# Optimization experiments

Hardware: AMD Instinct MI355X
Metric: run time of the kernel (lower is better)

Reference implementation:

```python
import jax, jax.numpy as jnp
import numpy as np

V = 1000      # output_dim (vocab)
H = 512       # hidden_dim
D = 512       # input_dim == d_model of MHA
HEADS = 8
DK = D // HEADS
MEM = 512     # memory_len
BS = 128      # batch
TMAX = 160    # max decode steps (== max(output_lens))


def setup_inputs() -> dict:
    key = jax.random.key(0)
    ks = jax.random.split(key, 16)
    s = 0.05
    f = lambda k, shape: jax.random.normal(k, shape, jnp.float32) * s
    memory = jax.random.normal(ks[0], (MEM, BS, D), jnp.float32)
    lens = jnp.sort(jax.random.randint(ks[1], (BS,), 1, TMAX + 1))[::-1]
    lens = lens.at[0].set(TMAX)  # torch runs max(output_lens) steps; pin to TMAX
    return dict(
        memory=memory,
        emb=f(ks[2], (V, H)),
        Wq=f(ks[3], (D, 2 * H)), bq=f(ks[4], (D,)),
        Wk=f(ks[5], (D, D)), bk=f(ks[6], (D,)),
        Wv=f(ks[7], (D, D)), bv=f(ks[8], (D,)),
        W_ih=f(ks[9], (3 * H, D)), W_hh=f(ks[10], (3 * H, H)),
        b_ih=f(ks[11], (3 * H,)), b_hh=f(ks[12], (3 * H,)),
        Wfc=f(ks[13], (V, H)), bfc=f(ks[14], (V,)),
        output_lens=lens,
    )


def _forward(memory, emb, Wq, bq, Wk, bk, Wv, bv, W_ih, W_hh, b_ih, b_hh, Wfc, bfc, output_lens):
    mem_len, bs, _ = memory.shape
    scale = 1.0 / np.sqrt(DK)
    # Precompute key/value projections once (memory is constant over decode steps).
    # (mem_len, bs, D) -> (bs, heads, mem_len, dk)
    kp = (memory @ Wk.T + bk).reshape(mem_len, bs, HEADS, DK).transpose(1, 2, 0, 3)
    vp = (memory @ Wv.T + bv).reshape(mem_len, bs, HEADS, DK).transpose(1, 2, 0, 3)

    def step(carry, i):
        out, hid = carry  # (bs, V), (bs, H)
        tok = jnp.argmax(out, axis=-1)                 # greedy feedback (annotations=None)
        q = jnp.concatenate([emb[tok], hid], axis=-1) @ Wq.T + bq  # (bs, D)
        qh = q.reshape(bs, HEADS, DK)
        att = jax.nn.softmax(jnp.einsum('bhd,bhmd->bhm', qh, kp) * scale, axis=-1)
        ctx = jnp.einsum('bhm,bhmd->bhd', att, vp).reshape(bs, D)
        # GRU cell (PyTorch gate order: r, z, n)
        gi = ctx @ W_ih.T + b_ih
        gh = hid @ W_hh.T + b_hh
        ir, iz, inn = jnp.split(gi, 3, axis=-1)
        hr, hz, hn = jnp.split(gh, 3, axis=-1)
        r = jax.nn.sigmoid(ir + hr)
        z = jax.nn.sigmoid(iz + hz)
        n = jnp.tanh(inn + r * hn)
        h_new = (1.0 - z) * n + z * hid
        o_new = h_new @ Wfc.T + bfc
        # Ragged masking: torch truncates finished batch items; each item is
        # independent, so masking the recorded outputs is equivalent.
        run = (i < output_lens)[:, None]
        ys = (jnp.where(run, o_new, 0.0),
              jnp.where(run, h_new, 0.0),
              jnp.where(run, att.mean(axis=1), 0.0))
        return (o_new, h_new), ys

    init = (jnp.zeros((bs, V), jnp.float32), jnp.zeros((bs, H), jnp.float32))
    _, (outputs, hiddens, scores) = jax.lax.scan(step, init, jnp.arange(TMAX))
    return outputs, hiddens, scores  # (T,bs,V), (T,bs,H), (T,bs,mem_len)


def reference(memory, emb, Wq, bq, Wk, bk, Wv, bv, W_ih, W_hh, b_ih, b_hh, Wfc, bfc, output_lens):
    return _forward(memory, emb, Wq, bq, Wk, bk, Wv, bv, W_ih, W_hh, b_ih, b_hh, Wfc, bfc, output_lens)
```

## Files before the change

kernel.cpp:

```cpp
#include <hip/hip_runtime.h>
#include <hip/hip_fp16.h>
#include <math.h>

__global__ __launch_bounds__(256) void kv_proj(
    const float* __restrict__ mem, const float* __restrict__ W,
    const float* __restrict__ bias, __half* __restrict__ outp) {
  __shared__ float As[32][68];
  __shared__ float Bs[32][68];
  int gid = blockIdx.x;
  int jt = gid & 7, mt = (gid >> 3) & 7, b = gid >> 6;
  int t = threadIdx.x;
  int lm = t >> 2;
  int kq = (t & 3) * 8;
  int tx = t & 15, ty = t >> 4;
  float acc[4][4];
  #pragma unroll
  for (int r = 0; r < 4; ++r)
    #pragma unroll
    for (int c = 0; c < 4; ++c) acc[r][c] = 0.f;
  const float* Arow = mem + (size_t)(mt * 64 + lm) * 65536 + (size_t)b * 512 + kq;
  const float* Brow = W + (size_t)(jt * 64 + lm) * 512 + kq;
  for (int k0 = 0; k0 < 512; k0 += 32) {
    float4 a0 = *(const float4*)(Arow + k0);
    float4 a1 = *(const float4*)(Arow + k0 + 4);
    float4 b0 = *(const float4*)(Brow + k0);
    float4 b1 = *(const float4*)(Brow + k0 + 4);
    As[kq + 0][lm] = a0.x; As[kq + 1][lm] = a0.y; As[kq + 2][lm] = a0.z; As[kq + 3][lm] = a0.w;
    As[kq + 4][lm] = a1.x; As[kq + 5][lm] = a1.y; As[kq + 6][lm] = a1.z; As[kq + 7][lm] = a1.w;
    Bs[kq + 0][lm] = b0.x; Bs[kq + 1][lm] = b0.y; Bs[kq + 2][lm] = b0.z; Bs[kq + 3][lm] = b0.w;
    Bs[kq + 4][lm] = b1.x; Bs[kq + 5][lm] = b1.y; Bs[kq + 6][lm] = b1.z; Bs[kq + 7][lm] = b1.w;
    __syncthreads();
    #pragma unroll
    for (int k = 0; k < 32; ++k) {
      float4 av = *(const float4*)&As[k][ty * 4];
      float4 bv = *(const float4*)&Bs[k][tx * 4];
      float ar[4] = {av.x, av.y, av.z, av.w};
      float br[4] = {bv.x, bv.y, bv.z, bv.w};
      #pragma unroll
      for (int r = 0; r < 4; ++r)
        #pragma unroll
        for (int c = 0; c < 4; ++c) acc[r][c] = fmaf(ar[r], br[c], acc[r][c]);
    }
    __syncthreads();
  }
  float4 bb = *(const float4*)(bias + jt * 64 + tx * 4);
  #pragma unroll
  for (int r = 0; r < 4; ++r) {
    int m = mt * 64 + ty * 4 + r;
    __half2 p0 = __floats2half2_rn(acc[r][0] + bb.x, acc[r][1] + bb.y);
    __half2 p1 = __floats2half2_rn(acc[r][2] + bb.z, acc[r][3] + bb.w);
    union { uint2 u; __half2 h[2]; } W2;
    W2.h[0] = p0; W2.h[1] = p1;
    *(uint2*)(outp + (((size_t)b * 8 + jt) * 512 + m) * 64 + tx * 4) = W2.u;
  }
}

__global__ __launch_bounds__(256) void kv_projT(
    const float* __restrict__ mem, const float* __restrict__ W,
    const float* __restrict__ bias, __half* __restrict__ outp) {
  __shared__ float As[32][68];
  __shared__ float Bs[32][68];
  int gid = blockIdx.x;
  int jt = gid & 7, mt = (gid >> 3) & 7, b = gid >> 6;
  int t = threadIdx.x;
  int lm = t >> 2;
  int kq = (t & 3) * 8;
  int tx = t & 15, ty = t >> 4;
  float acc[4][4];
  #pragma unroll
  for (int r = 0; r < 4; ++r)
    #pragma unroll
    for (int c = 0; c < 4; ++c) acc[r][c] = 0.f;
  const float* Arow = mem + (size_t)(mt * 64 + lm) * 65536 + (size_t)b * 512 + kq;
  const float* Brow = W + (size_t)(jt * 64 + lm) * 512 + kq;
  for (int k0 = 0; k0 < 512; k0 += 32) {
    float4 a0 = *(const float4*)(Arow + k0);
    float4 a1 = *(const float4*)(Arow + k0 + 4);
    float4 b0 = *(const float4*)(Brow + k0);
    float4 b1 = *(const float4*)(Brow + k0 + 4);
    As[kq + 0][lm] = a0.x; As[kq + 1][lm] = a0.y; As[kq + 2][lm] = a0.z; As[kq + 3][lm] = a0.w;
    As[kq + 4][lm] = a1.x; As[kq + 5][lm] = a1.y; As[kq + 6][lm] = a1.z; As[kq + 7][lm] = a1.w;
    Bs[kq + 0][lm] = b0.x; Bs[kq + 1][lm] = b0.y; Bs[kq + 2][lm] = b0.z; Bs[kq + 3][lm] = b0.w;
    Bs[kq + 4][lm] = b1.x; Bs[kq + 5][lm] = b1.y; Bs[kq + 6][lm] = b1.z; Bs[kq + 7][lm] = b1.w;
    __syncthreads();
    #pragma unroll
    for (int k = 0; k < 32; ++k) {
      float4 av = *(const float4*)&As[k][ty * 4];
      float4 bv = *(const float4*)&Bs[k][tx * 4];
      float ar[4] = {av.x, av.y, av.z, av.w};
      float br[4] = {bv.x, bv.y, bv.z, bv.w};
      #pragma unroll
      for (int r = 0; r < 4; ++r)
        #pragma unroll
        for (int c = 0; c < 4; ++c) acc[r][c] = fmaf(ar[r], br[c], acc[r][c]);
    }
    __syncthreads();
  }
  float4 bb = *(const float4*)(bias + jt * 64 + tx * 4);
  float bc[4] = {bb.x, bb.y, bb.z, bb.w};
  #pragma unroll
  for (int r = 0; r < 4; ++r) {
    int m = mt * 64 + ty * 4 + r;
    #pragma unroll
    for (int c = 0; c < 4; ++c) {
      int d = tx * 4 + c;
      outp[((size_t)(b * 8 + jt) * 64 + d) * 512 + m] = __float2half_rn(acc[r][c] + bc[c]);
    }
  }
}

__global__ __launch_bounds__(256) void e2_kernel(
    const float* __restrict__ emb, const float* __restrict__ Wq,
    const float* __restrict__ bq, float* __restrict__ E2) {
  __shared__ float As[32][68];
  __shared__ float Bs[32][68];
  int gid = blockIdx.x;
  int jt = gid & 7, mt = gid >> 3;
  int t = threadIdx.x;
  int lm = t >> 2;
  int kq = (t & 3) * 8;
  int tx = t & 15, ty = t >> 4;
  float acc[4][4];
  #pragma unroll
  for (int r = 0; r < 4; ++r)
    #pragma unroll
    for (int c = 0; c < 4; ++c) acc[r][c] = 0.f;
  int v = mt * 64 + lm;
  bool aok = v < 1000;
  const float* Arow = emb + (size_t)v * 512 + kq;
  const float* Brow = Wq + (size_t)(jt * 64 + lm) * 1024 + kq;
  for (int k0 = 0; k0 < 512; k0 += 32) {
    float4 a0, a1;
    if (aok) {
      a0 = *(const float4*)(Arow + k0);
      a1 = *(const float4*)(Arow + k0 + 4);
    } else {
      a0 = make_float4(0.f, 0.f, 0.f, 0.f);
      a1 = make_float4(0.f, 0.f, 0.f, 0.f);
    }
    float4 b0 = *(const float4*)(Brow + k0);
    float4 b1 = *(const float4*)(Brow + k0 + 4);
    As[kq + 0][lm] = a0.x; As[kq + 1][lm] = a0.y; As[kq + 2][lm] = a0.z; As[kq + 3][lm] = a0.w;
    As[kq + 4][lm] = a1.x; As[kq + 5][lm] = a1.y; As[kq + 6][lm] = a1.z; As[kq + 7][lm] = a1.w;
    Bs[kq + 0][lm] = b0.x; Bs[kq + 1][lm] = b0.y; Bs[kq + 2][lm] = b0.z; Bs[kq + 3][lm] = b0.w;
    Bs[kq + 4][lm] = b1.x; Bs[kq + 5][lm] = b1.y; Bs[kq + 6][lm] = b1.z; Bs[kq + 7][lm] = b1.w;
    __syncthreads();
    #pragma unroll
    for (int k = 0; k < 32; ++k) {
      float4 av = *(const float4*)&As[k][ty * 4];
      float4 bv = *(const float4*)&Bs[k][tx * 4];
      float ar[4] = {av.x, av.y, av.z, av.w};
      float br[4] = {bv.x, bv.y, bv.z, bv.w};
      #pragma unroll
      for (int r = 0; r < 4; ++r)
        #pragma unroll
        for (int c = 0; c < 4; ++c) acc[r][c] = fmaf(ar[r], br[c], acc[r][c]);
    }
    __syncthreads();
  }
  float4 bb = *(const float4*)(bq + jt * 64 + tx * 4);
  float bc[4] = {bb.x, bb.y, bb.z, bb.w};
  #pragma unroll
  for (int r = 0; r < 4; ++r) {
    int vv = mt * 64 + ty * 4 + r;
    if (vv < 1000) {
      #pragma unroll
      for (int c = 0; c < 4; ++c)
        E2[(size_t)vv * 512 + jt * 64 + tx * 4 + c] = acc[r][c] + bc[c];
    }
  }
}

__global__ __launch_bounds__(256) void init_kernel(float* __restrict__ h0,
                                                   float* __restrict__ qh,
                                                   unsigned long long* __restrict__ packed) {
  int t = threadIdx.x + blockIdx.x * blockDim.x;
  for (int i = t; i < 128 * 512; i += blockDim.x * gridDim.x) {
    h0[i] = 0.f;
    qh[i] = 0.f;
  }
  if (t < 128) packed[t] = (0x80000000ull << 32) | 0xFFFFFFFFull;
}

__global__ __launch_bounds__(256) void attn_fused(
    const __half* __restrict__ kpT, const __half* __restrict__ vp,
    const float* __restrict__ E2, const float* __restrict__ qh,
    const unsigned long long* __restrict__ packed,
    float* __restrict__ ctx, float* __restrict__ att_buf) {
  int b = blockIdx.x >> 3, hd = blockIdx.x & 7;
  __shared__ float qs[64];
  __shared__ float att[512];
  __shared__ __align__(16) float red[16][68];
  __shared__ float rmax[4], rsum[4];
  __shared__ int tok_s;
  int t = threadIdx.x;
  if (t == 0) tok_s = (int)(0xFFFFFFFFu - (unsigned int)(packed[b] & 0xFFFFFFFFull));
  __syncthreads();
  int tok = tok_s;
  if (t < 64)
    qs[t] = qh[(size_t)b * 512 + hd * 64 + t] + E2[(size_t)tok * 512 + hd * 64 + t];
  __syncthreads();

  const __half* Kb = kpT + (size_t)(b * 8 + hd) * 32768;
  float s0 = 0.f, s1 = 0.f;
  {
    int m2 = 2 * t;
    #pragma unroll 16
    for (int d = 0; d < 64; ++d) {
      __half2 kk = *(const __half2*)(Kb + (size_t)d * 512 + m2);
      float2 kf = __half22float2(kk);
      float qd = qs[d];
      s0 = fmaf(qd, kf.x, s0);
      s1 = fmaf(qd, kf.y, s1);
    }
    s0 *= 0.125f;
    s1 *= 0.125f;
  }
  float mx = fmaxf(s0, s1);
  #pragma unroll
  for (int o = 32; o > 0; o >>= 1) mx = fmaxf(mx, __shfl_xor(mx, o));
  if ((t & 63) == 0) rmax[t >> 6] = mx;
  __syncthreads();
  mx = fmaxf(fmaxf(rmax[0], rmax[1]), fmaxf(rmax[2], rmax[3]));
  float e0 = expf(s0 - mx), e1 = expf(s1 - mx);
  float sm = e0 + e1;
  #pragma unroll
  for (int o = 32; o > 0; o >>= 1) sm += __shfl_xor(sm, o);
  if ((t & 63) == 0) rsum[t >> 6] = sm;
  __syncthreads();
  sm = rsum[0] + rsum[1] + rsum[2] + rsum[3];
  float inv = 1.f / sm;
  float a0 = e0 * inv, a1 = e1 * inv;
  att[2 * t] = a0;
  att[2 * t + 1] = a1;
  *(float2*)(att_buf + (size_t)(b * 8 + hd) * 512 + 2 * t) = make_float2(a0, a1);
  __syncthreads();

  const __half* Vb = vp + (size_t)(b * 8 + hd) * 32768;
  {
    int dsl = (t & 15) * 4, g = t >> 4;
    float c0 = 0.f, c1 = 0.f, c2 = 0.f, c3 = 0.f;
    #pragma unroll 8
    for (int m = g; m < 512; m += 16) {
      union { uint2 u; __half2 h[2]; } U;
      U.u = *(const uint2*)(Vb + (size_t)m * 64 + dsl);
      float2 f01 = __half22float2(U.h[0]);
      float2 f23 = __half22float2(U.h[1]);
      float am = att[m];
      c0 = fmaf(am, f01.x, c0);
      c1 = fmaf(am, f01.y, c1);
      c2 = fmaf(am, f23.x, c2);
      c3 = fmaf(am, f23.y, c3);
    }
    red[g][dsl + 0] = c0;
    red[g][dsl + 1] = c1;
    red[g][dsl + 2] = c2;
    red[g][dsl + 3] = c3;
  }
  __syncthreads();
  if (t < 64) {
    float cc = 0.f;
    #pragma unroll
    for (int g2 = 0; g2 < 16; ++g2) cc += red[g2][t];
    ctx[(size_t)b * 512 + hd * 64 + t] = cc;
  }
}

__global__ __launch_bounds__(256) void gru_kernel(
    const float* __restrict__ W_ih, const float* __restrict__ W_hh,
    const float* __restrict__ b_ih, const float* __restrict__ b_hh,
    const float* __restrict__ ctx, const float* __restrict__ h_prev,
    float* __restrict__ h_new, const float* __restrict__ att_buf,
    const int* __restrict__ lens, float* __restrict__ out_hid,
    float* __restrict__ out_sc, unsigned long long* __restrict__ packed,
    int step) {
  __shared__ float cs[8][512];
  __shared__ float hs[8][512];
  int bi = blockIdx.x;
  int t = threadIdx.x;
  if (bi >= 256) {
    int sb = bi - 256;
    if (sb == 0 && t < 128) packed[t] = 0ull;
    #pragma unroll
    for (int i = 0; i < 4; ++i) {
      int flat = sb * 1024 + i * 256 + t;
      int bb = flat >> 9, m = flat & 511;
      float sum = 0.f;
      #pragma unroll
      for (int h = 0; h < 8; ++h) sum += att_buf[(size_t)(bb * 8 + h) * 512 + m];
      float val = sum * 0.125f;
      out_sc[(size_t)step * 65536 + flat] = (step < lens[bb]) ? val : 0.f;
    }
    return;
  }
  int bt = bi >> 4, jt = bi & 15;
  #pragma unroll
  for (int i = 0; i < 16; ++i) {
    int flat = i * 256 + t;
    int lb = flat >> 9, k = flat & 511;
    cs[lb][k] = ctx[(size_t)(bt * 8 + lb) * 512 + k];
    hs[lb][k] = h_prev[(size_t)(bt * 8 + lb) * 512 + k];
  }
  __syncthreads();
  int lb = t >> 5, j = (jt << 5) + (t & 31);
  int b = bt * 8 + lb;
  float air = b_ih[j], aiz = b_ih[512 + j], ain = b_ih[1024 + j];
  float ahr = b_hh[j], ahz = b_hh[512 + j], ahn = b_hh[1024 + j];
  const float* c = cs[lb];
  const float* hh = hs[lb];
  const float* wi0 = W_ih + (size_t)j * 512;
  const float* wi1 = W_ih + (size_t)(512 + j) * 512;
  const float* wi2 = W_ih + (size_t)(1024 + j) * 512;
  const float* wh0 = W_hh + (size_t)j * 512;
  const float* wh1 = W_hh + (size_t)(512 + j) * 512;
  const float* wh2 = W_hh + (size_t)(1024 + j) * 512;
  #pragma unroll 2
  for (int k = 0; k < 512; k += 4) {
    float4 wa = *(const float4*)(wi0 + k);
    float4 wb = *(const float4*)(wi1 + k);
    float4 wc = *(const float4*)(wi2 + k);
    float4 wd = *(const float4*)(wh0 + k);
    float4 we = *(const float4*)(wh1 + k);
    float4 wf = *(const float4*)(wh2 + k);
    float c0 = c[k], c1 = c[k + 1], c2 = c[k + 2], c3 = c[k + 3];
    float h0 = hh[k], h1 = hh[k + 1], h2 = hh[k + 2], h3 = hh[k + 3];
    air = fmaf(c0, wa.x, air); air = fmaf(c1, wa.y, air); air = fmaf(c2, wa.z, air); air = fmaf(c3, wa.w, air);
    aiz = fmaf(c0, wb.x, aiz); aiz = fmaf(c1, wb.y, aiz); aiz = fmaf(c2, wb.z, aiz); aiz = fmaf(c3, wb.w, aiz);
    ain = fmaf(c0, wc.x, ain); ain = fmaf(c1, wc.y, ain); ain = fmaf(c2, wc.z, ain); ain = fmaf(c3, wc.w, ain);
    ahr = fmaf(h0, wd.x, ahr); ahr = fmaf(h1, wd.y, ahr); ahr = fmaf(h2, wd.z, ahr); ahr = fmaf(h3, wd.w, ahr);
    ahz = fmaf(h0, we.x, ahz); ahz = fmaf(h1, we.y, ahz); ahz = fmaf(h2, we.z, ahz); ahz = fmaf(h3, we.w, ahz);
    ahn = fmaf(h0, wf.x, ahn); ahn = fmaf(h1, wf.y, ahn); ahn = fmaf(h2, wf.z, ahn); ahn = fmaf(h3, wf.w, ahn);
  }
  float r = 1.f / (1.f + expf(-(air + ahr)));
  float z = 1.f / (1.f + expf(-(aiz + ahz)));
  float n = tanhf(fmaf(r, ahn, ain));
  float hp = hh[j];
  float hv = (1.f - z) * n + z * hp;
  h_new[(size_t)b * 512 + j] = hv;
  out_hid[(size_t)step * 65536 + (size_t)b * 512 + j] = (step < lens[b]) ? hv : 0.f;
}

__global__ __launch_bounds__(256) void logits_kernel(
    const float* __restrict__ Wfc, const float* __restrict__ bfc,
    const float* __restrict__ h_new, const int* __restrict__ lens,
    float* __restrict__ out_o, unsigned long long* __restrict__ packed,
    const float* __restrict__ Wq, float* __restrict__ qh, int step) {
  __shared__ float hs[8][512];
  int bi = blockIdx.x;
  int t = threadIdx.x;
  int bt = bi >> 4, vt = bi & 15;
  #pragma unroll
  for (int i = 0; i < 16; ++i) {
    int flat = i * 256 + t;
    int lb = flat >> 9, k = flat & 511;
    hs[lb][k] = h_new[(size_t)(bt * 8 + lb) * 512 + k];
  }
  __syncthreads();
  int lb = t >> 5, vv = t & 31;
  int b = bt * 8 + lb;
  const float* a = hs[lb];
  int run = step < lens[b];
  float bestv = -1e30f;
  int besti = 0;
  #pragma unroll
  for (int r = 0; r < 2; ++r) {
    int v = vt * 64 + r * 32 + vv;
    if (v < 1000) {
      float acc = bfc[v];
      const float* wrow = Wfc + (size_t)v * 512;
      #pragma unroll 4
      for (int k = 0; k < 512; k += 4) {
        float4 w = *(const float4*)(wrow + k);
        acc = fmaf(a[k + 0], w.x, acc);
        acc = fmaf(a[k + 1], w.y, acc);
        acc = fmaf(a[k + 2], w.z, acc);
        acc = fmaf(a[k + 3], w.w, acc);
      }
      out_o[(size_t)step * 128000 + (size_t)b * 1000 + v] = run ? acc : 0.f;
      if (acc > bestv) { bestv = acc; besti = v; }
    }
  }
  #pragma unroll
  for (int o = 16; o > 0; o >>= 1) {
    float ov = __shfl_xor(bestv, o);
    int oi = __shfl_xor(besti, o);
    if (ov > bestv || (ov == bestv && oi < besti)) { bestv = ov; besti = oi; }
  }
  if (vv == 0) {
    unsigned int fb = __float_as_uint(bestv);
    fb = (fb & 0x80000000u) ? ~fb : (fb | 0x80000000u);
    unsigned long long key =
        ((unsigned long long)fb << 32) | (unsigned long long)(0xFFFFFFFFu - (unsigned int)besti);
    atomicMax(packed + b, key);
  }

  {
    int jq = vt * 32 + (t & 31);
    const float* wrow = Wq + (size_t)jq * 1024 + 512;
    float acc = 0.f;
    #pragma unroll 4
    for (int k = 0; k < 512; k += 4) {
      float4 w = *(const float4*)(wrow + k);
      acc = fmaf(a[k + 0], w.x, acc);
      acc = fmaf(a[k + 1], w.y, acc);
      acc = fmaf(a[k + 2], w.z, acc);
      acc = fmaf(a[k + 3], w.w, acc);
    }
    qh[(size_t)b * 512 + jq] = acc;
  }
}

extern "C" void kernel_launch(void* const* d_in, const int* in_sizes, int n_in,
                              void* d_out, int out_size, void* d_ws, size_t ws_size,
                              hipStream_t stream) {
  const float* memory = (const float*)d_in[0];
  const float* emb    = (const float*)d_in[1];
  const float* Wq     = (const float*)d_in[2];
  const float* bq     = (const float*)d_in[3];
  const float* Wk     = (const float*)d_in[4];
  const float* bk     = (const float*)d_in[5];
  const float* Wv     = (const float*)d_in[6];
  const float* bv     = (const float*)d_in[7];
  const float* W_ih   = (const float*)d_in[8];
  const float* W_hh   = (const float*)d_in[9];
  const float* b_ih   = (const float*)d_in[10];
  const float* b_hh   = (const float*)d_in[11];
  const float* Wfc    = (const float*)d_in[12];
  const float* bfc    = (const float*)d_in[13];
  const int* lens     = (const int*)d_in[14];

  __half* kpT = (__half*)d_ws;
  __half* vp  = kpT + 33554432;
  float* ctx     = (float*)(vp + 33554432);
  float* h0      = ctx + 65536;
  float* h1      = h0 + 65536;
  float* qh      = h1 + 65536;
  float* E2      = qh + 65536;
  float* att_buf = E2 + 512000;
  unsigned long long* packed = (unsigned long long*)(att_buf + 524288);

  float* out   = (float*)d_out;
  float* out_o = out;
  float* out_h = out + 20480000;
  float* out_s = out_h + 10485760;

  kv_projT<<<8192, 256, 0, stream>>>(memory, Wk, bk, kpT);
  kv_proj<<<8192, 256, 0, stream>>>(memory, Wv, bv, vp);
  e2_kernel<<<128, 256, 0, stream>>>(emb, Wq, bq, E2);
  init_kernel<<<64, 256, 0, stream>>>(h0, qh, packed);

  for (int t = 0; t < 160; ++t) {
    float* hp = (t & 1) ? h1 : h0;
    float* hn = (t & 1) ? h0 : h1;
    attn_fused<<<1024, 256, 0, stream>>>(kpT, vp, E2, qh, packed, ctx, att_buf);
    gru_kernel<<<320, 256, 0, stream>>>(W_ih, W_hh, b_ih, b_hh, ctx, hp, hn,
                                        att_buf, lens, out_h, out_s, packed, t);
    logits_kernel<<<256, 256, 0, stream>>>(Wfc, bfc, hn, lens, out_o, packed, Wq, qh, t);
  }
}
```

Before: 25.94 ms.

## Fuse decode loop into one persistent cooperative kernel with grid syncs

Replaces the 480 per-step kernel launches (attention, GRU, logits) with a single cooperative persistent kernel of 512 blocks that loops over the 160 steps and separates phases with grid-wide syncs. Each block handles two batch-head attention tiles per step, and a subset of blocks then runs the GRU and logits phases. The goal is to remove launch overhead and inter-kernel gaps. The cost is lower parallelism in the attention phase (1024 tiles on 512 blocks) and grid.sync overhead. The old multi-kernel loop stays as a fallback if the cooperative launch fails.

```diff
diff --git a/kernel.cpp b/kernel.cpp
--- a/kernel.cpp
+++ b/kernel.cpp
@@ -1,6 +1,9 @@
 #include <hip/hip_runtime.h>
 #include <hip/hip_fp16.h>
+#include <hip/hip_cooperative_groups.h>
 #include <math.h>
+
+namespace cg = cooperative_groups;
 
 __global__ __launch_bounds__(256) void kv_proj(
     const float* __restrict__ mem, const float* __restrict__ W,
@@ -200,7 +203,6 @@
   if (t < 64)
     qs[t] = qh[(size_t)b * 512 + hd * 64 + t] + E2[(size_t)tok * 512 + hd * 64 + t];
   __syncthreads();
-
   const __half* Kb = kpT + (size_t)(b * 8 + hd) * 32768;
   float s0 = 0.f, s1 = 0.f;
   {
@@ -235,7 +237,6 @@
   att[2 * t + 1] = a1;
   *(float2*)(att_buf + (size_t)(b * 8 + hd) * 512 + 2 * t) = make_float2(a0, a1);
   __syncthreads();
-
   const __half* Vb = vp + (size_t)(b * 8 + hd) * 32768;
   {
     int dsl = (t & 15) * 4, g = t >> 4;
@@ -393,7 +394,6 @@
         ((unsigned long long)fb << 32) | (unsigned long long)(0xFFFFFFFFu - (unsigned int)besti);
     atomicMax(packed + b, key);
   }
-
   {
     int jq = vt * 32 + (t & 31);
     const float* wrow = Wq + (size_t)jq * 1024 + 512;
@@ -407,6 +407,249 @@
       acc = fmaf(a[k + 3], w.w, acc);
     }
     qh[(size_t)b * 512 + jq] = acc;
+  }
+}
+
+__global__ __launch_bounds__(256, 2) void decode_kernel(
+    const __half* __restrict__ kpT, const __half* __restrict__ vp,
+    const float* __restrict__ E2, float* __restrict__ qh,
+    float* __restrict__ h0, float* __restrict__ h1,
+    float* __restrict__ ctx, float* __restrict__ att_buf,
+    unsigned long long* __restrict__ packed,
+    const float* __restrict__ W_ih, const float* __restrict__ W_hh,
+    const float* __restrict__ b_ih, const float* __restrict__ b_hh,
+    const float* __restrict__ Wfc, const float* __restrict__ bfc,
+    const float* __restrict__ Wq, const int* __restrict__ lens,
+    float* __restrict__ out_o, float* __restrict__ out_h,
+    float* __restrict__ out_s) {
+  cg::grid_group grid = cg::this_grid();
+  __shared__ __align__(16) float smem[8192];
+  __shared__ int tok_s;
+  int g = blockIdx.x;
+  int t = threadIdx.x;
+
+  {
+    int idx = g * 256 + t;
+    if (idx < 65536) { h0[idx] = 0.f; qh[idx] = 0.f; }
+    if (idx < 128) packed[idx] = (0x80000000ull << 32) | 0xFFFFFFFFull;
+  }
+  grid.sync();
+
+  for (int step = 0; step < 160; ++step) {
+    const float* hp = (step & 1) ? h1 : h0;
+    float* hn = (step & 1) ? h0 : h1;
+
+    #pragma unroll 1
+    for (int p = 0; p < 2; ++p) {
+      int id = (g << 1) | p;
+      int b = id >> 3, hd = id & 7;
+      float* qs = smem;
+      float* att = smem + 64;
+      float (*red)[68] = reinterpret_cast<float(*)[68]>(smem + 576);
+      float* rmax = smem + 1664;
+      float* rsum = smem + 1668;
+
+      if (t == 0) tok_s = (int)(0xFFFFFFFFu - (unsigned int)(packed[b] & 0xFFFFFFFFull));
+      __syncthreads();
+      int tok = tok_s;
+      if (t < 64)
+        qs[t] = qh[(size_t)b * 512 + hd * 64 + t] + E2[(size_t)tok * 512 + hd * 64 + t];
+      __syncthreads();
+
+      const __half* Kb = kpT + (size_t)(b * 8 + hd) * 32768;
+      float s0 = 0.f, s1 = 0.f;
+      {
+        int m2 = 2 * t;
+        #pragma unroll 16
+        for (int d = 0; d < 64; ++d) {
+          __half2 kk = *(const __half2*)(Kb + (size_t)d * 512 + m2);
+          float2 kf = __half22float2(kk);
+          float qd = qs[d];
+          s0 = fmaf(qd, kf.x, s0);
+          s1 = fmaf(qd, kf.y, s1);
+        }
+        s0 *= 0.125f;
+        s1 *= 0.125f;
+      }
+      float mx = fmaxf(s0, s1);
+      #pragma unroll
+      for (int o = 32; o > 0; o >>= 1) mx = fmaxf(mx, __shfl_xor(mx, o));
+      if ((t & 63) == 0) rmax[t >> 6] = mx;
+      __syncthreads();
+      mx = fmaxf(fmaxf(rmax[0], rmax[1]), fmaxf(rmax[2], rmax[3]));
+      float e0 = expf(s0 - mx), e1 = expf(s1 - mx);
+      float sm = e0 + e1;
+      #pragma unroll
+      for (int o = 32; o > 0; o >>= 1) sm += __shfl_xor(sm, o);
+      if ((t & 63) == 0) rsum[t >> 6] = sm;
+      __syncthreads();
+      sm = rsum[0] + rsum[1] + rsum[2] + rsum[3];
+      float inv = 1.f / sm;
+      float a0 = e0 * inv, a1 = e1 * inv;
+      att[2 * t] = a0;
+      att[2 * t + 1] = a1;
+      *(float2*)(att_buf + (size_t)(b * 8 + hd) * 512 + 2 * t) = make_float2(a0, a1);
+      __syncthreads();
+
+      const __half* Vb = vp + (size_t)(b * 8 + hd) * 32768;
+      {
+        int dsl = (t & 15) * 4, g4 = t >> 4;
+        float c0 = 0.f, c1 = 0.f, c2 = 0.f, c3 = 0.f;
+        #pragma unroll 8
+        for (int m = g4; m < 512; m += 16) {
+          union { uint2 u; __half2 h[2]; } U;
+          U.u = *(const uint2*)(Vb + (size_t)m * 64 + dsl);
+          float2 f01 = __half22float2(U.h[0]);
+          float2 f23 = __half22float2(U.h[1]);
+          float am = att[m];
+          c0 = fmaf(am, f01.x, c0);
+          c1 = fmaf(am, f01.y, c1);
+          c2 = fmaf(am, f23.x, c2);
+          c3 = fmaf(am, f23.y, c3);
+        }
+        red[g4][dsl + 0] = c0;
+        red[g4][dsl + 1] = c1;
+        red[g4][dsl + 2] = c2;
+        red[g4][dsl + 3] = c3;
+      }
+      __syncthreads();
+      if (t < 64) {
+        float cc = 0.f;
+        #pragma unroll
+        for (int g2 = 0; g2 < 16; ++g2) cc += red[g2][t];
+        ctx[(size_t)b * 512 + hd * 64 + t] = cc;
+      }
+      __syncthreads();
+    }
+    grid.sync();
+
+    if (g < 256) {
+      float (*cs)[512] = reinterpret_cast<float(*)[512]>(smem);
+      float (*hs)[512] = reinterpret_cast<float(*)[512]>(smem + 4096);
+      int bt = g >> 4, jt = g & 15;
+      #pragma unroll
+      for (int i = 0; i < 16; ++i) {
+        int flat = i * 256 + t;
+        int lb = flat >> 9, k = flat & 511;
+        cs[lb][k] = ctx[(size_t)(bt * 8 + lb) * 512 + k];
+        hs[lb][k] = hp[(size_t)(bt * 8 + lb) * 512 + k];
+      }
+      __syncthreads();
+      int lb = t >> 5, j = (jt << 5) + (t & 31);
+      int b = bt * 8 + lb;
+      float air = b_ih[j], aiz = b_ih[512 + j], ain = b_ih[1024 + j];
+      float ahr = b_hh[j], ahz = b_hh[512 + j], ahn = b_hh[1024 + j];
+      const float* c = cs[lb];
+      const float* hh = hs[lb];
+      const float* wi0 = W_ih + (size_t)j * 512;
+      const float* wi1 = W_ih + (size_t)(512 + j) * 512;
+      const float* wi2 = W_ih + (size_t)(1024 + j) * 512;
+      const float* wh0 = W_hh + (size_t)j * 512;
+      const float* wh1 = W_hh + (size_t)(512 + j) * 512;
+      const float* wh2 = W_hh + (size_t)(1024 + j) * 512;
+      #pragma unroll 2
+      for (int k = 0; k < 512; k += 4) {
+        float4 wa = *(const float4*)(wi0 + k);
+        float4 wb = *(const float4*)(wi1 + k);
+        float4 wc = *(const float4*)(wi2 + k);
+        float4 wd = *(const float4*)(wh0 + k);
+        float4 we = *(const float4*)(wh1 + k);
+        float4 wf = *(const float4*)(wh2 + k);
+        float c0 = c[k], c1 = c[k + 1], c2 = c[k + 2], c3 = c[k + 3];
+        float h0v = hh[k], h1v = hh[k + 1], h2v = hh[k + 2], h3v = hh[k + 3];
+        air = fmaf(c0, wa.x, air); air = fmaf(c1, wa.y, air); air = fmaf(c2, wa.z, air); air = fmaf(c3, wa.w, air);
+        aiz = fmaf(c0, wb.x, aiz); aiz = fmaf(c1, wb.y, aiz); aiz = fmaf(c2, wb.z, aiz); aiz = fmaf(c3, wb.w, aiz);
+        ain = fmaf(c0, wc.x, ain); ain = fmaf(c1, wc.y, ain); ain = fmaf(c2, wc.z, ain); ain = fmaf(c3, wc.w, ain);
+        ahr = fmaf(h0v, wd.x, ahr); ahr = fmaf(h1v, wd.y, ahr); ahr = fmaf(h2v, wd.z, ahr); ahr = fmaf(h3v, wd.w, ahr);
+        ahz = fmaf(h0v, we.x, ahz); ahz = fmaf(h1v, we.y, ahz); ahz = fmaf(h2v, we.z, ahz); ahz = fmaf(h3v, we.w, ahz);
+        ahn = fmaf(h0v, wf.x, ahn); ahn = fmaf(h1v, wf.y, ahn); ahn = fmaf(h2v, wf.z, ahn); ahn = fmaf(h3v, wf.w, ahn);
+      }
+      float r = 1.f / (1.f + expf(-(air + ahr)));
+      float z = 1.f / (1.f + expf(-(aiz + ahz)));
+      float n = tanhf(fmaf(r, ahn, ain));
+      float hpv = hh[j];
+      float hv = (1.f - z) * n + z * hpv;
+      hn[(size_t)b * 512 + j] = hv;
+      out_h[(size_t)step * 65536 + (size_t)b * 512 + j] = (step < lens[b]) ? hv : 0.f;
+    } else if (g < 320) {
+      int sb = g - 256;
+      if (sb == 0 && t < 128) packed[t] = 0ull;
+      #pragma unroll
+      for (int i = 0; i < 4; ++i) {
+        int flat = sb * 1024 + i * 256 + t;
+        int bb = flat >> 9, m = flat & 511;
+        float sum = 0.f;
+        #pragma unroll
+        for (int h = 0; h < 8; ++h) sum += att_buf[(size_t)(bb * 8 + h) * 512 + m];
+        float val = sum * 0.125f;
+        out_s[(size_t)step * 65536 + flat] = (step < lens[bb]) ? val : 0.f;
+      }
+    }
+    grid.sync();
+
+    if (g < 256) {
+      float (*hs)[512] = reinterpret_cast<float(*)[512]>(smem);
+      int bt = g >> 4, vt = g & 15;
+      #pragma unroll
+      for (int i = 0; i < 16; ++i) {
+        int flat = i * 256 + t;
+        int lb = flat >> 9, k = flat & 511;
+        hs[lb][k] = hn[(size_t)(bt * 8 + lb) * 512 + k];
+      }
+      __syncthreads();
+      int lb = t >> 5, vv = t & 31;
+      int b = bt * 8 + lb;
+      const float* a = hs[lb];
+      int run = step < lens[b];
+      float bestv = -1e30f;
+      int besti = 0;
+      #pragma unroll
+      for (int r = 0; r < 2; ++r) {
+        int v = vt * 64 + r * 32 + vv;
+        if (v < 1000) {
+          float acc = bfc[v];
+          const float* wrow = Wfc + (size_t)v * 512;
+          #pragma unroll 4
+          for (int k = 0; k < 512; k += 4) {
+            float4 w = *(const float4*)(wrow + k);
+            acc = fmaf(a[k + 0], w.x, acc);
+            acc = fmaf(a[k + 1], w.y, acc);
+            acc = fmaf(a[k + 2], w.z, acc);
+            acc = fmaf(a[k + 3], w.w, acc);
+          }
+          out_o[(size_t)step * 128000 + (size_t)b * 1000 + v] = run ? acc : 0.f;
+          if (acc > bestv) { bestv = acc; besti = v; }
+        }
+      }
+      #pragma unroll
+      for (int o = 16; o > 0; o >>= 1) {
+        float ov = __shfl_xor(bestv, o);
+        int oi = __shfl_xor(besti, o);
+        if (ov > bestv || (ov == bestv && oi < besti)) { bestv = ov; besti = oi; }
+      }
+      if (vv == 0) {
+        unsigned int fb = __float_as_uint(bestv);
+        fb = (fb & 0x80000000u) ? ~fb : (fb | 0x80000000u);
+        unsigned long long key =
+            ((unsigned long long)fb << 32) | (unsigned long long)(0xFFFFFFFFu - (unsigned int)besti);
+        atomicMax(packed + b, key);
+      }
+      {
+        int jq = vt * 32 + (t & 31);
+        const float* wrow = Wq + (size_t)jq * 1024 + 512;
+        float acc = 0.f;
+        #pragma unroll 4
+        for (int k = 0; k < 512; k += 4) {
+          float4 w = *(const float4*)(wrow + k);
+          acc = fmaf(a[k + 0], w.x, acc);
+          acc = fmaf(a[k + 1], w.y, acc);
+          acc = fmaf(a[k + 2], w.z, acc);
+          acc = fmaf(a[k + 3], w.w, acc);
+        }
+        qh[(size_t)b * 512 + jq] = acc;
+      }
+    }
+    grid.sync();
   }
 }
 
@@ -447,14 +690,25 @@
   kv_projT<<<8192, 256, 0, stream>>>(memory, Wk, bk, kpT);
   kv_proj<<<8192, 256, 0, stream>>>(memory, Wv, bv, vp);
   e2_kernel<<<128, 256, 0, stream>>>(emb, Wq, bq, E2);
-  init_kernel<<<64, 256, 0, stream>>>(h0, qh, packed);
-
-  for (int t = 0; t < 160; ++t) {
-    float* hp = (t & 1) ? h1 : h0;
-    float* hn = (t & 1) ? h0 : h1;
-    attn_fused<<<1024, 256, 0, stream>>>(kpT, vp, E2, qh, packed, ctx, att_buf);
-    gru_kernel<<<320, 256, 0, stream>>>(W_ih, W_hh, b_ih, b_hh, ctx, hp, hn,
-                                        att_buf, lens, out_h, out_s, packed, t);
-    logits_kernel<<<256, 256, 0, stream>>>(Wfc, bfc, hn, lens, out_o, packed, Wq, qh, t);
-  }
-}
+
+  void* args[] = {
+      (void*)&kpT, (void*)&vp, (void*)&E2, (void*)&qh, (void*)&h0, (void*)&h1,
+      (void*)&ctx, (void*)&att_buf, (void*)&packed,
+      (void*)&W_ih, (void*)&W_hh, (void*)&b_ih, (void*)&b_hh,
+      (void*)&Wfc, (void*)&bfc, (void*)&Wq, (void*)&lens,
+      (void*)&out_o, (void*)&out_h, (void*)&out_s};
+  hipError_t err = hipLaunchCooperativeKernel((void*)decode_kernel, dim3(512),
+                                              dim3(256), args, 0, stream);
+  if (err != hipSuccess) {
+    init_kernel<<<64, 256, 0, stream>>>(h0, qh, packed);
+    for (int t = 0; t < 160; ++t) {
+      float* hp = (t & 1) ? h1 : h0;
+      float* hn = (t & 1) ? h0 : h1;
+      attn_fused<<<1024, 256, 0, stream>>>(kpT, vp, E2, qh, packed, ctx, att_buf);
+      gru_kernel<<<320, 256, 0, stream>>>(W_ih, W_hh, b_ih, b_hh, ctx, hp, hn,
+                                          att_buf, lens, out_h, out_s, packed, t);
+      logits_kernel<<<256, 256, 0, stream>>>(Wfc, bfc, hn, lens, out_o, packed, Wq,
+                                             qh, t);
+    }
+  }
+}
```

Measured after the change: 55.43 ms. 114% more time.

## Fuse logits, argmax and query projection into per-batch attention kernel

Applied to the files above, without the earlier changes.

The logits/argmax/query-projection work for step t-1 moves into the start of the next step's attention kernel. That kernel now runs one 512-thread block per batch item and covers all heads, so the argmax is resolved in shared memory instead of through global atomics on a packed buffer. The attention-score mean is also folded into this kernel, which drops the att_buf round trip and a launch per step. The cost is that each block recomputes the full Wfc and Wq matvecs for its batch item, so only 128 blocks run with heavy per-block weight streaming. That means less parallelism than the previous 1024-block attention and 256-block logits grids.

```diff
diff --git a/kernel.cpp b/kernel.cpp
--- a/kernel.cpp
+++ b/kernel.cpp
@@ -171,128 +171,154 @@
   }
 }
 
-__global__ __launch_bounds__(256) void init_kernel(float* __restrict__ h0,
-                                                   float* __restrict__ qh,
-                                                   unsigned long long* __restrict__ packed) {
+__global__ __launch_bounds__(256) void init_kernel(float* __restrict__ h0) {
   int t = threadIdx.x + blockIdx.x * blockDim.x;
-  for (int i = t; i < 128 * 512; i += blockDim.x * gridDim.x) {
-    h0[i] = 0.f;
-    qh[i] = 0.f;
-  }
-  if (t < 128) packed[t] = (0x80000000ull << 32) | 0xFFFFFFFFull;
-}
-
-__global__ __launch_bounds__(256) void attn_fused(
+  for (int i = t; i < 128 * 512; i += blockDim.x * gridDim.x) h0[i] = 0.f;
+}
+
+__global__ __launch_bounds__(512) void attn_step(
     const __half* __restrict__ kpT, const __half* __restrict__ vp,
-    const float* __restrict__ E2, const float* __restrict__ qh,
-    const unsigned long long* __restrict__ packed,
-    float* __restrict__ ctx, float* __restrict__ att_buf) {
-  int b = blockIdx.x >> 3, hd = blockIdx.x & 7;
-  __shared__ float qs[64];
-  __shared__ float att[512];
-  __shared__ __align__(16) float red[16][68];
-  __shared__ float rmax[4], rsum[4];
+    const float* __restrict__ E2, const float* __restrict__ Wfc,
+    const float* __restrict__ bfc, const float* __restrict__ Wq,
+    const float* __restrict__ h_prev, const int* __restrict__ lens,
+    float* __restrict__ out_o, float* __restrict__ out_s,
+    float* __restrict__ ctx, int step) {
+  int b = blockIdx.x;
+  int t = threadIdx.x;
+  __shared__ float hs[512];
+  __shared__ float qs[512];
+  __shared__ __align__(16) float att[8][512];
+  __shared__ float redv[8];
+  __shared__ int redi[8];
   __shared__ int tok_s;
-  int t = threadIdx.x;
-  if (t == 0) tok_s = (int)(0xFFFFFFFFu - (unsigned int)(packed[b] & 0xFFFFFFFFull));
+
+  if (step > 0) {
+    hs[t] = h_prev[(size_t)b * 512 + t];
+    __syncthreads();
+    int run = (step - 1) < lens[b];
+    float bestv = -1e30f;
+    int besti = 0;
+    #pragma unroll
+    for (int s = 0; s < 2; ++s) {
+      int v = t + s * 512;
+      if (v < 1000) {
+        float acc = bfc[v];
+        const float* wrow = Wfc + (size_t)v * 512;
+        #pragma unroll 4
+        for (int k = 0; k < 512; k += 4) {
+          float4 w = *(const float4*)(wrow + k);
+          acc = fmaf(hs[k + 0], w.x, acc);
+          acc = fmaf(hs[k + 1], w.y, acc);
+          acc = fmaf(hs[k + 2], w.z, acc);
+          acc = fmaf(hs[k + 3], w.w, acc);
+        }
+        out_o[(size_t)(step - 1) * 128000 + (size_t)b * 1000 + v] = run ? acc : 0.f;
+        if (acc > bestv) { bestv = acc; besti = v; }
+      }
+    }
+    #pragma unroll
+    for (int o = 32; o > 0; o >>= 1) {
+      float ov = __shfl_xor(bestv, o);
+      int oi = __shfl_xor(besti, o);
+      if (ov > bestv || (ov == bestv && oi < besti)) { bestv = ov; besti = oi; }
+    }
+    if ((t & 63) == 0) { redv[t >> 6] = bestv; redi[t >> 6] = besti; }
+    float qhv = 0.f;
+    {
+      const float* wrow = Wq + (size_t)t * 1024 + 512;
+      #pragma unroll 4
+      for (int k = 0; k < 512; k += 4) {
+        float4 w = *(const float4*)(wrow + k);
+        qhv = fmaf(hs[k + 0], w.x, qhv);
+        qhv = fmaf(hs[k + 1], w.y, qhv);
+        qhv = fmaf(hs[k + 2], w.z, qhv);
+        qhv = fmaf(hs[k + 3], w.w, qhv);
+      }
+    }
+    __syncthreads();
+    if (t == 0) {
+      float bv = redv[0];
+      int bi = redi[0];
+      #pragma unroll
+      for (int i = 1; i < 8; ++i)
+        if (redv[i] > bv || (redv[i] == bv && redi[i] < bi)) { bv = redv[i]; bi = redi[i]; }
+      tok_s = bi;
+    }
+    __syncthreads();
+    if (step >= 160) return;
+    qs[t] = qhv + E2[(size_t)tok_s * 512 + t];
+    __syncthreads();
+  } else {
+    qs[t] = E2[t];
+    __syncthreads();
+  }
+
+  int hd = t >> 6, lane = t & 63;
+  const __half* Kb = kpT + (size_t)(b * 8 + hd) * 32768;
+  float s0[4], s1[4];
+  #pragma unroll
+  for (int i = 0; i < 4; ++i) { s0[i] = 0.f; s1[i] = 0.f; }
+  for (int d = 0; d < 64; ++d) {
+    float qd = qs[hd * 64 + d];
+    const __half* kr = Kb + (size_t)d * 512;
+    #pragma unroll
+    for (int i = 0; i < 4; ++i) {
+      __half2 kk = *(const __half2*)(kr + 2 * (lane + 64 * i));
+      float2 kf = __half22float2(kk);
+      s0[i] = fmaf(qd, kf.x, s0[i]);
+      s1[i] = fmaf(qd, kf.y, s1[i]);
+    }
+  }
+  float mx = -1e30f;
+  #pragma unroll
+  for (int i = 0; i < 4; ++i) {
+    s0[i] *= 0.125f;
+    s1[i] *= 0.125f;
+    mx = fmaxf(mx, fmaxf(s0[i], s1[i]));
+  }
+  #pragma unroll
+  for (int o = 32; o > 0; o >>= 1) mx = fmaxf(mx, __shfl_xor(mx, o));
+  float e0[4], e1[4], sm = 0.f;
+  #pragma unroll
+  for (int i = 0; i < 4; ++i) {
+    e0[i] = expf(s0[i] - mx);
+    e1[i] = expf(s1[i] - mx);
+    sm += e0[i] + e1[i];
+  }
+  #pragma unroll
+  for (int o = 32; o > 0; o >>= 1) sm += __shfl_xor(sm, o);
+  float inv = 1.f / sm;
+  #pragma unroll
+  for (int i = 0; i < 4; ++i)
+    *(float2*)&att[hd][2 * (lane + 64 * i)] = make_float2(e0[i] * inv, e1[i] * inv);
   __syncthreads();
-  int tok = tok_s;
-  if (t < 64)
-    qs[t] = qh[(size_t)b * 512 + hd * 64 + t] + E2[(size_t)tok * 512 + hd * 64 + t];
-  __syncthreads();
-
-  const __half* Kb = kpT + (size_t)(b * 8 + hd) * 32768;
-  float s0 = 0.f, s1 = 0.f;
+
   {
-    int m2 = 2 * t;
-    #pragma unroll 16
-    for (int d = 0; d < 64; ++d) {
-      __half2 kk = *(const __half2*)(Kb + (size_t)d * 512 + m2);
-      float2 kf = __half22float2(kk);
-      float qd = qs[d];
-      s0 = fmaf(qd, kf.x, s0);
-      s1 = fmaf(qd, kf.y, s1);
-    }
-    s0 *= 0.125f;
-    s1 *= 0.125f;
-  }
-  float mx = fmaxf(s0, s1);
-  #pragma unroll
-  for (int o = 32; o > 0; o >>= 1) mx = fmaxf(mx, __shfl_xor(mx, o));
-  if ((t & 63) == 0) rmax[t >> 6] = mx;
-  __syncthreads();
-  mx = fmaxf(fmaxf(rmax[0], rmax[1]), fmaxf(rmax[2], rmax[3]));
-  float e0 = expf(s0 - mx), e1 = expf(s1 - mx);
-  float sm = e0 + e1;
-  #pragma unroll
-  for (int o = 32; o > 0; o >>= 1) sm += __shfl_xor(sm, o);
-  if ((t & 63) == 0) rsum[t >> 6] = sm;
-  __syncthreads();
-  sm = rsum[0] + rsum[1] + rsum[2] + rsum[3];
-  float inv = 1.f / sm;
-  float a0 = e0 * inv, a1 = e1 * inv;
-  att[2 * t] = a0;
-  att[2 * t + 1] = a1;
-  *(float2*)(att_buf + (size_t)(b * 8 + hd) * 512 + 2 * t) = make_float2(a0, a1);
-  __syncthreads();
+    float sum2 = 0.f;
+    #pragma unroll
+    for (int h2 = 0; h2 < 8; ++h2) sum2 += att[h2][t];
+    out_s[(size_t)step * 65536 + (size_t)b * 512 + t] =
+        (step < lens[b]) ? sum2 * 0.125f : 0.f;
+  }
 
   const __half* Vb = vp + (size_t)(b * 8 + hd) * 32768;
-  {
-    int dsl = (t & 15) * 4, g = t >> 4;
-    float c0 = 0.f, c1 = 0.f, c2 = 0.f, c3 = 0.f;
-    #pragma unroll 8
-    for (int m = g; m < 512; m += 16) {
-      union { uint2 u; __half2 h[2]; } U;
-      U.u = *(const uint2*)(Vb + (size_t)m * 64 + dsl);
-      float2 f01 = __half22float2(U.h[0]);
-      float2 f23 = __half22float2(U.h[1]);
-      float am = att[m];
-      c0 = fmaf(am, f01.x, c0);
-      c1 = fmaf(am, f01.y, c1);
-      c2 = fmaf(am, f23.x, c2);
-      c3 = fmaf(am, f23.y, c3);
-    }
-    red[g][dsl + 0] = c0;
-    red[g][dsl + 1] = c1;
-    red[g][dsl + 2] = c2;
-    red[g][dsl + 3] = c3;
-  }
-  __syncthreads();
-  if (t < 64) {
-    float cc = 0.f;
-    #pragma unroll
-    for (int g2 = 0; g2 < 16; ++g2) cc += red[g2][t];
-    ctx[(size_t)b * 512 + hd * 64 + t] = cc;
-  }
+  float cc = 0.f;
+  #pragma unroll 8
+  for (int m = 0; m < 512; ++m)
+    cc = fmaf(att[hd][m], __half2float(Vb[(size_t)m * 64 + lane]), cc);
+  ctx[(size_t)b * 512 + hd * 64 + lane] = cc;
 }
 
 __global__ __launch_bounds__(256) void gru_kernel(
     const float* __restrict__ W_ih, const float* __restrict__ W_hh,
     const float* __restrict__ b_ih, const float* __restrict__ b_hh,
     const float* __restrict__ ctx, const float* __restrict__ h_prev,
-    float* __restrict__ h_new, const float* __restrict__ att_buf,
-    const int* __restrict__ lens, float* __restrict__ out_hid,
-    float* __restrict__ out_sc, unsigned long long* __restrict__ packed,
-    int step) {
+    float* __restrict__ h_new, const int* __restrict__ lens,
+    float* __restrict__ out_hid, int step) {
   __shared__ float cs[8][512];
   __shared__ float hs[8][512];
   int bi = blockIdx.x;
   int t = threadIdx.x;
-  if (bi >= 256) {
-    int sb = bi - 256;
-    if (sb == 0 && t < 128) packed[t] = 0ull;
-    #pragma unroll
-    for (int i = 0; i < 4; ++i) {
-      int flat = sb * 1024 + i * 256 + t;
-      int bb = flat >> 9, m = flat & 511;
-      float sum = 0.f;
-      #pragma unroll
-      for (int h = 0; h < 8; ++h) sum += att_buf[(size_t)(bb * 8 + h) * 512 + m];
-      float val = sum * 0.125f;
-      out_sc[(size_t)step * 65536 + flat] = (step < lens[bb]) ? val : 0.f;
-    }
-    return;
-  }
   int bt = bi >> 4, jt = bi & 15;
   #pragma unroll
   for (int i = 0; i < 16; ++i) {
@@ -340,76 +366,6 @@
   out_hid[(size_t)step * 65536 + (size_t)b * 512 + j] = (step < lens[b]) ? hv : 0.f;
 }
 
-__global__ __launch_bounds__(256) void logits_kernel(
-    const float* __restrict__ Wfc, const float* __restrict__ bfc,
-    const float* __restrict__ h_new, const int* __restrict__ lens,
-    float* __restrict__ out_o, unsigned long long* __restrict__ packed,
-    const float* __restrict__ Wq, float* __restrict__ qh, int step) {
-  __shared__ float hs[8][512];
-  int bi = blockIdx.x;
-  int t = threadIdx.x;
-  int bt = bi >> 4, vt = bi & 15;
-  #pragma unroll
-  for (int i = 0; i < 16; ++i) {
-    int flat = i * 256 + t;
-    int lb = flat >> 9, k = flat & 511;
-    hs[lb][k] = h_new[(size_t)(bt * 8 + lb) * 512 + k];
-  }
-  __syncthreads();
-  int lb = t >> 5, vv = t & 31;
-  int b = bt * 8 + lb;
-  const float* a = hs[lb];
-  int run = step < lens[b];
-  float bestv = -1e30f;
-  int besti = 0;
-  #pragma unroll
-  for (int r = 0; r < 2; ++r) {
-    int v = vt * 64 + r * 32 + vv;
-    if (v < 1000) {
-      float acc = bfc[v];
-      const float* wrow = Wfc + (size_t)v * 512;
-      #pragma unroll 4
-      for (int k = 0; k < 512; k += 4) {
-        float4 w = *(const float4*)(wrow + k);
-        acc = fmaf(a[k + 0], w.x, acc);
-        acc = fmaf(a[k + 1], w.y, acc);
-        acc = fmaf(a[k + 2], w.z, acc);
-        acc = fmaf(a[k + 3], w.w, acc);
-      }
-      out_o[(size_t)step * 128000 + (size_t)b * 1000 + v] = run ? acc : 0.f;
-      if (acc > bestv) { bestv = acc; besti = v; }
-    }
-  }
-  #pragma unroll
-  for (int o = 16; o > 0; o >>= 1) {
-    float ov = __shfl_xor(bestv, o);
-    int oi = __shfl_xor(besti, o);
-    if (ov > bestv || (ov == bestv && oi < besti)) { bestv = ov; besti = oi; }
-  }
-  if (vv == 0) {
-    unsigned int fb = __float_as_uint(bestv);
-    fb = (fb & 0x80000000u) ? ~fb : (fb | 0x80000000u);
-    unsigned long long key =
-        ((unsigned long long)fb << 32) | (unsigned long long)(0xFFFFFFFFu - (unsigned int)besti);
-    atomicMax(packed + b, key);
-  }
-
-  {
-    int jq = vt * 32 + (t & 31);
-    const float* wrow = Wq + (size_t)jq * 1024 + 512;
-    float acc = 0.f;
-    #pragma unroll 4
-    for (int k = 0; k < 512; k += 4) {
-      float4 w = *(const float4*)(wrow + k);
-      acc = fmaf(a[k + 0], w.x, acc);
-      acc = fmaf(a[k + 1], w.y, acc);
-      acc = fmaf(a[k + 2], w.z, acc);
-      acc = fmaf(a[k + 3], w.w, acc);
-    }
-    qh[(size_t)b * 512 + jq] = acc;
-  }
-}
-
 extern "C" void kernel_launch(void* const* d_in, const int* in_sizes, int n_in,
                               void* d_out, int out_size, void* d_ws, size_t ws_size,
                               hipStream_t stream) {
@@ -434,10 +390,7 @@
   float* ctx     = (float*)(vp + 33554432);
   float* h0      = ctx + 65536;
   float* h1      = h0 + 65536;
-  float* qh      = h1 + 65536;
-  float* E2      = qh + 65536;
-  float* att_buf = E2 + 512000;
-  unsigned long long* packed = (unsigned long long*)(att_buf + 524288);
+  float* E2      = h1 + 65536;
 
   float* out   = (float*)d_out;
   float* out_o = out;
@@ -447,14 +400,17 @@
   kv_projT<<<8192, 256, 0, stream>>>(memory, Wk, bk, kpT);
   kv_proj<<<8192, 256, 0, stream>>>(memory, Wv, bv, vp);
   e2_kernel<<<128, 256, 0, stream>>>(emb, Wq, bq, E2);
-  init_kernel<<<64, 256, 0, stream>>>(h0, qh, packed);
+  init_kernel<<<64, 256, 0, stream>>>(h0);
 
   for (int t = 0; t < 160; ++t) {
+    const float* hprev_attn = (t == 0) ? h0 : (((t - 1) & 1) ? h0 : h1);
+    attn_step<<<128, 512, 0, stream>>>(kpT, vp, E2, Wfc, bfc, Wq, hprev_attn,
+                                       lens, out_o, out_s, ctx, t);
     float* hp = (t & 1) ? h1 : h0;
     float* hn = (t & 1) ? h0 : h1;
-    attn_fused<<<1024, 256, 0, stream>>>(kpT, vp, E2, qh, packed, ctx, att_buf);
-    gru_kernel<<<320, 256, 0, stream>>>(W_ih, W_hh, b_ih, b_hh, ctx, hp, hn,
-                                        att_buf, lens, out_h, out_s, packed, t);
-    logits_kernel<<<256, 256, 0, stream>>>(Wfc, bfc, hn, lens, out_o, packed, Wq, qh, t);
-  }
-}
+    gru_kernel<<<256, 256, 0, stream>>>(W_ih, W_hh, b_ih, b_hh, ctx, hp, hn,
+                                        lens, out_h, t);
+  }
+  attn_step<<<128, 512, 0, stream>>>(kpT, vp, E2, Wfc, bfc, Wq, h0, lens,
+                                     out_o, out_s, ctx, 160);
+}
```

Result: slower. 33.85 ms (+30.5%).
